# Performance work log

Measured on AMD Instinct MI355X. Metric: run time of the kernel, lower is better.

## Reference

```python
import jax, jax.numpy as jnp
import numpy as np

NN = 128  # number of neighbors (self.nn in the torch module)


def _safe_cdist(A, B):
    # Euclidean pairwise distance with grad-safe sqrt at exact zeros
    sq = (jnp.sum(A * A, -1)[..., :, None]
          + jnp.sum(B * B, -1)[..., None, :]
          - 2.0 * jnp.matmul(A, jnp.swapaxes(B, -1, -2)))
    sq = jnp.maximum(sq, 0.0)
    pos = sq > 0
    return jnp.where(pos, jnp.sqrt(jnp.where(pos, sq, 1.0)), 0.0)


def _kernel(A, B, lv, av):
    # a * exp(-cdist(A/l, B/l) / sqrt(D))
    d = _safe_cdist(A / lv, B / lv) / np.sqrt(A.shape[-1])
    return av * jnp.exp(-d)


def setup_inputs() -> dict:
    key = jax.random.key(0)
    k = jax.random.split(key, 5)
    B, N, D, O = 1024, 100000, 256, 1
    return {
        "x": jax.random.normal(k[0], (B, D), jnp.float32),
        "trainX": jax.random.normal(k[1], (N, D), jnp.float32),
        "trainy": jax.random.normal(k[2], (N, O), jnp.float32),
        "noise": jax.random.normal(k[3], (B, NN, O), jnp.float32),
        "l": jnp.zeros((), jnp.float32),
        "a": jnp.zeros((), jnp.float32),
        "ymean": jnp.zeros((), jnp.float32),
    }


def reference(x, trainX, trainy, noise, l, a, ymean):
    lv = jnp.exp(l)
    av = jnp.exp(a)
    # [B, N] distances, kNN retrieval (eval path: topk of nn, no self-exclusion)
    dists = _safe_cdist(x / lv, trainX / lv)
    _, neighbors = jax.lax.top_k(-dists, NN)          # smallest distances
    nX = trainX[neighbors]                            # [B, NN, D]
    ny = trainy[neighbors] + 0.01 * noise - ymean     # [B, NN, O]
    auto = _kernel(nX, nX, lv, av)                    # [B, NN, NN]
    autoCov = jnp.linalg.inv(auto)                    # batched 128x128 inverse
    crossCov = _kernel(x[:, None, :], nX, lv, av)     # [B, 1, NN]
    kW = crossCov @ autoCov                           # [B, 1, NN]
    y = kW @ ny                                       # [B, 1, O]
    yVar = av * jnp.ones(x.shape[0], x.dtype) - jnp.squeeze(
        kW @ jnp.swapaxes(crossCov, -1, -2))          # [B]
    return (jnp.squeeze(y + ymean, 1), yVar)
```

## Files before the change

kernel.cpp:

```cpp
#include <hip/hip_runtime.h>
#include <math.h>
#include <stdint.h>

#define B_SZ    1024
#define N_TRAIN 100000
#define N_PAD   100096
#define D_DIM   256
#define NN      128
#define KSEL    256
#define CAP     2048
#define NSAMP   1024
#define SRANK   8

typedef unsigned short u16;
typedef unsigned long long u64;
typedef __attribute__((ext_vector_type(8))) short short8v;
typedef __attribute__((ext_vector_type(4))) float f32x4;

__device__ inline u16 f2bf(float f) {
    unsigned u = __float_as_uint(f);
    return (u16)((u + 0x7FFFu + ((u >> 16) & 1u)) >> 16);
}
__device__ inline float bf2f(u16 h) { return __uint_as_float((unsigned)h << 16); }

__global__ __launch_bounds__(256) void k0_norms(const float* __restrict__ trainX,
                                                const float* __restrict__ x,
                                                float* __restrict__ tt,
                                                float* __restrict__ xx) {
    int wave = (blockIdx.x * blockDim.x + threadIdx.x) >> 6;
    int lane = threadIdx.x & 63;
    if (wave >= N_TRAIN + B_SZ) return;
    const float* row = (wave < N_TRAIN) ? (trainX + (size_t)wave * D_DIM)
                                        : (x + (size_t)(wave - N_TRAIN) * D_DIM);
    float4 v = ((const float4*)row)[lane];
    float s = v.x*v.x + v.y*v.y + v.z*v.z + v.w*v.w;
    for (int off = 32; off; off >>= 1) s += __shfl_down(s, off, 64);
    if (lane == 0) { if (wave < N_TRAIN) tt[wave] = s; else xx[wave - N_TRAIN] = s; }
}

__global__ __launch_bounds__(256) void kcv(const float* __restrict__ src,
                                           u16* __restrict__ dst, int n4) {
    int stride = gridDim.x * 256;
    for (int i = blockIdx.x * 256 + threadIdx.x; i < n4; i += stride) {
        float4 v = ((const float4*)src)[i];
        u64 p = (u64)f2bf(v.x) | ((u64)f2bf(v.y) << 16)
              | ((u64)f2bf(v.z) << 32) | ((u64)f2bf(v.w) << 48);
        ((u64*)dst)[i] = p;
    }
}

__global__ __launch_bounds__(256) void kcv2(const float* __restrict__ src,
                                            u16* __restrict__ dstH,
                                            u16* __restrict__ dstL, int n4) {
    int stride = gridDim.x * 256;
    for (int i = blockIdx.x * 256 + threadIdx.x; i < n4; i += stride) {
        float4 v = ((const float4*)src)[i];
        u16 h0 = f2bf(v.x), h1 = f2bf(v.y), h2 = f2bf(v.z), h3 = f2bf(v.w);
        u16 l0 = f2bf(v.x - bf2f(h0)), l1 = f2bf(v.y - bf2f(h1));
        u16 l2 = f2bf(v.z - bf2f(h2)), l3 = f2bf(v.w - bf2f(h3));
        ((u64*)dstH)[i] = (u64)h0 | ((u64)h1 << 16) | ((u64)h2 << 32) | ((u64)h3 << 48);
        ((u64*)dstL)[i] = (u64)l0 | ((u64)l1 << 16) | ((u64)l2 << 32) | ((u64)l3 << 48);
    }
}

__global__ __launch_bounds__(256) void k1m(const u16* __restrict__ Ah,
                                           const u16* __restrict__ Bh,
                                           const float* __restrict__ xx,
                                           const float* __restrict__ tt,
                                           u16* __restrict__ distu,
                                           int row0, int nrows) {
    __shared__ u16 Als[4][128][8];
    __shared__ u16 Bls[4][128][8];
    const int tid = threadIdx.x;
    const int lane = tid & 63, wv = tid >> 6;
    const int wr = wv >> 1, wc = wv & 1;
    const int ib = blockIdx.y * 128;
    const size_t jb = (size_t)blockIdx.x * 128;

    f32x4 acc[4][4];
    #pragma unroll
    for (int m = 0; m < 4; ++m)
        #pragma unroll
        for (int n = 0; n < 4; ++n)
            #pragma unroll
            for (int r = 0; r < 4; ++r) acc[m][n][r] = 0.f;

    for (int k0 = 0; k0 < D_DIM; k0 += 32) {
        #pragma unroll
        for (int r = 0; r < 2; ++r) {
            int c = tid + r * 256;
            int row = c >> 2, ks = c & 3;
            uint4 va = make_uint4(0, 0, 0, 0);
            if (ib + row < nrows)
                va = *(const uint4*)(Ah + (size_t)(row0 + ib + row) * D_DIM + k0 + ks * 8);
            *(uint4*)(&Als[ks][row][0]) = va;
            uint4 vb = make_uint4(0, 0, 0, 0);
            if (jb + row < N_TRAIN)
                vb = *(const uint4*)(Bh + (jb + row) * D_DIM + k0 + ks * 8);
            *(uint4*)(&Bls[ks][row][0]) = vb;
        }
        __syncthreads();
        const int ksl = lane >> 4, li = lane & 15;
        short8v a[4], b[4];
        #pragma unroll
        for (int m = 0; m < 4; ++m)
            a[m] = *(const short8v*)&Als[ksl][wr * 64 + m * 16 + li][0];
        #pragma unroll
        for (int n = 0; n < 4; ++n)
            b[n] = *(const short8v*)&Bls[ksl][wc * 64 + n * 16 + li][0];
        #pragma unroll
        for (int m = 0; m < 4; ++m)
            #pragma unroll
            for (int n = 0; n < 4; ++n)
                acc[m][n] = __builtin_amdgcn_mfma_f32_16x16x32_bf16(a[m], b[n], acc[m][n], 0, 0, 0);
        __syncthreads();
    }
    const int li = lane & 15, lh = lane >> 4;
    float ttv[4]; int cols[4];
    #pragma unroll
    for (int n = 0; n < 4; ++n) {
        cols[n] = (int)jb + wc * 64 + n * 16 + li;
        ttv[n] = (cols[n] < N_TRAIN) ? tt[cols[n]] : 0.f;
    }
    #pragma unroll
    for (int m = 0; m < 4; ++m)
        #pragma unroll
        for (int r = 0; r < 4; ++r) {
            int rl = ib + wr * 64 + m * 16 + lh * 4 + r;
            if (rl >= nrows) continue;
            float xi = xx[row0 + rl];
            u64 pk = 0;
            #pragma unroll
            for (int n = 0; n < 4; ++n) {
                u16 code = 0xFFFFu;
                if (cols[n] < N_TRAIN)
                    code = f2bf(fmaxf(xi + ttv[n] - 2.0f * acc[m][n][r], 0.f));
                pk |= (u64)code << (16 * n);
            }
            *(u64*)(distu + (size_t)rl * N_PAD + jb + wc * 64 + li * 4) = pk;
        }
}

__device__ inline void bitonicU64N(u64* a, int tid, int NE) {
    for (int ks = 2; ks <= NE; ks <<= 1)
        for (int js = ks >> 1; js > 0; js >>= 1) {
            __syncthreads();
            for (int e = tid; e < NE; e += 256) {
                int p = e ^ js;
                if (p > e) {
                    u64 A = a[e], B = a[p];
                    if ((A > B) == ((e & ks) == 0)) { a[e] = B; a[p] = A; }
                }
            }
        }
    __syncthreads();
}
__device__ inline void bitonicU16N(u16* a, int tid, int NE) {
    for (int ks = 2; ks <= NE; ks <<= 1)
        for (int js = ks >> 1; js > 0; js >>= 1) {
            __syncthreads();
            for (int e = tid; e < NE; e += 256) {
                int p = e ^ js;
                if (p > e) {
                    u16 A = a[e], B = a[p];
                    if ((A > B) == ((e & ks) == 0)) { a[e] = B; a[p] = A; }
                }
            }
        }
    __syncthreads();
}

__global__ __launch_bounds__(256) void k2_select(const u16* __restrict__ distu, int row0,
                                                 const float* __restrict__ x,
                                                 const float* __restrict__ trainX,
                                                 const float* __restrict__ xx,
                                                 const float* __restrict__ tt,
                                                 int* __restrict__ nidx,
                                                 float* __restrict__ nsq) {
    const int tid = threadIdx.x;
    const int b = row0 + blockIdx.x;
    const u16* row = distu + (size_t)blockIdx.x * N_PAD;
    const uint4* row8 = (const uint4*)row;
    __shared__ u64 buf[CAP];
    __shared__ int s_cnt;
    __shared__ int sIdx[KSEL];
    __shared__ float4 xs4[64];
    u16* samp = (u16*)buf;

    if (tid < NSAMP / 8) ((uint4*)samp)[tid] = row8[tid];
    __syncthreads();
    bitonicU16N(samp, tid, NSAMP);
    int Tc = (int)samp[SRANK];
    __syncthreads();

    int cnt = 0;
    for (int att = 0; att < 8; ++att) {
        if (tid == 0) s_cnt = 0;
        __syncthreads();
        for (int j8 = tid; j8 < N_PAD / 8; j8 += 256) {
            uint4 v = row8[j8];
            unsigned w_[4] = {v.x, v.y, v.z, v.w};
            #pragma unroll
            for (int c2 = 0; c2 < 4; ++c2) {
                #pragma unroll
                for (int hc = 0; hc < 2; ++hc) {
                    int code = (int)(hc ? (w_[c2] >> 16) : (w_[c2] & 0xFFFFu));
                    if (code < Tc) {
                        int p = atomicAdd(&s_cnt, 1);
                        if (p < CAP) buf[p] = ((u64)(unsigned)code << 32)
                                            | (unsigned)(j8 * 8 + c2 * 2 + hc);
                    }
                }
            }
        }
        __syncthreads();
        cnt = s_cnt;
        if (cnt >= KSEL && cnt <= CAP) break;
        Tc += (cnt < KSEL) ? 8 : -8;
        __syncthreads();
    }
    if (cnt > CAP) cnt = CAP;
    int NE = KSEL;
    while (NE < cnt) NE <<= 1;
    for (int i = tid; i < NE; i += 256) if (i >= cnt) buf[i] = ~0ull;
    __syncthreads();
    bitonicU64N(buf, tid, NE);
    {
        u64 e = buf[tid];
        int jraw = (e == ~0ull) ? 0 : (int)(e & 0xFFFFFFFFull);
        int base = (jraw >> 7) << 7, off = jraw & 127;
        sIdx[tid] = base + (off & 64) + ((off & 3) << 4) + ((off & 63) >> 2);
    }
    if (tid < 64) xs4[tid] = ((const float4*)(x + (size_t)b * D_DIM))[tid];
    __syncthreads();

    const int lane = tid & 63, wv = tid >> 6;
    const int ls = lane & 31;
    const float xxb = xx[b];
    for (int it = 0; it < KSEL / 8; ++it) {
        int c = it * 8 + wv * 2 + (lane >> 5);
        int j = sIdx[c];
        const float4* tr = (const float4*)(trainX + (size_t)j * D_DIM);
        float4 p1 = tr[ls * 2], p2 = tr[ls * 2 + 1];
        float4 q1 = xs4[ls * 2], q2 = xs4[ls * 2 + 1];
        float d = p1.x*q1.x + p1.y*q1.y + p1.z*q1.z + p1.w*q1.w
                + p2.x*q2.x + p2.y*q2.y + p2.z*q2.z + p2.w*q2.w;
        #pragma unroll
        for (int m = 1; m < 32; m <<= 1) d += __shfl_xor(d, m, 64);
        if (ls == 0) {
            float sq = fmaxf(xxb + tt[j] - 2.0f * d, 0.f);
            buf[c] = ((u64)__float_as_uint(sq) << 32) | (unsigned)j;
        }
    }
    __syncthreads();
    bitonicU64N(buf, tid, KSEL);
    if (tid < NN) {
        u64 e = buf[tid];
        nidx[(size_t)b * NN + tid] = (int)(e & 0xFFFFFFFFull);
        nsq[(size_t)b * NN + tid]  = __uint_as_float((unsigned)(e >> 32));
    }
}

__global__ __launch_bounds__(256, 2) void k3_solve(
    const u16* __restrict__ Bh, const u16* __restrict__ Bl,
    const float* __restrict__ trainy,
    const float* __restrict__ noise, const float* __restrict__ tt,
    const int* __restrict__ nidx, const float* __restrict__ nsq,
    const float* __restrict__ lp, const float* __restrict__ ap,
    const float* __restrict__ ymp, float* __restrict__ out) {

    __shared__ u16 Shi[128][40];
    __shared__ u16 Slo[128][40];
    __shared__ float pbuf[2][4][NN];
    __shared__ float diagb[2][4][4];
    __shared__ float yLds[NN], yfwd[NN], dvec[NN], wvec[NN];
    __shared__ int   idxs[NN];
    __shared__ float ttn[NN], c0v[NN];
    __shared__ float red[8];

    const int b = blockIdx.x;
    const int tid = threadIdx.x;
    const int lane = tid & 63, wv = tid >> 6;
    const int wr = wv >> 1, wc = wv & 1;
    const int lr = lane & 15, lq = lane >> 4;

    const float lv = expf(lp[0]);
    const float av = expf(ap[0]);
    const float ymean = ymp[0];
    const float sc = 1.0f / (lv * 16.0f);

    if (tid < NN) {
        int ix = nidx[(size_t)b * NN + tid];
        idxs[tid] = ix;
        ttn[tid] = tt[ix];
        float cc = av * expf(-sqrtf(nsq[(size_t)b * NN + tid]) * sc);
        c0v[tid] = cc;
        yLds[tid] = cc;
    }
    __syncthreads();

    f32x4 acc[4][4];
    #pragma unroll
    for (int m = 0; m < 4; ++m)
        #pragma unroll
        for (int n = 0; n < 4; ++n)
            #pragma unroll
            for (int r = 0; r < 4; ++r) acc[m][n][r] = 0.f;

    for (int c = 0; c < 8; ++c) {
        #pragma unroll
        for (int s = 0; s < 2; ++s) {
            int idx = tid + s * 256;
            int row = idx >> 2, kp = (idx & 3) << 3;
            size_t base = (size_t)idxs[row] * D_DIM + c * 32 + kp;
            *(uint4*)&Shi[row][kp] = *(const uint4*)(Bh + base);
            *(uint4*)&Slo[row][kp] = *(const uint4*)(Bl + base);
        }
        __syncthreads();
        {
            short8v ahi[4], bhi[4];
            #pragma unroll
            for (int m = 0; m < 4; ++m)
                ahi[m] = *(const short8v*)&Shi[wr * 64 + m * 16 + lr][lq * 8];
            #pragma unroll
            for (int n = 0; n < 4; ++n)
                bhi[n] = *(const short8v*)&Shi[wc * 64 + n * 16 + lr][lq * 8];
            #pragma unroll
            for (int m = 0; m < 4; ++m)
                #pragma unroll
                for (int n = 0; n < 4; ++n)
                    acc[m][n] = __builtin_amdgcn_mfma_f32_16x16x32_bf16(ahi[m], bhi[n], acc[m][n], 0, 0, 0);
            #pragma unroll
            for (int n = 0; n < 4; ++n) {
                short8v blo = *(const short8v*)&Slo[wc * 64 + n * 16 + lr][lq * 8];
                #pragma unroll
                for (int m = 0; m < 4; ++m)
                    acc[m][n] = __builtin_amdgcn_mfma_f32_16x16x32_bf16(ahi[m], blo, acc[m][n], 0, 0, 0);
            }
            #pragma unroll
            for (int m = 0; m < 4; ++m) {
                short8v alo = *(const short8v*)&Slo[wr * 64 + m * 16 + lr][lq * 8];
                #pragma unroll
                for (int n = 0; n < 4; ++n)
                    acc[m][n] = __builtin_amdgcn_mfma_f32_16x16x32_bf16(alo, bhi[n], acc[m][n], 0, 0, 0);
            }
        }
        __syncthreads();
    }

    float em[4][4][4];
    #pragma unroll
    for (int m = 0; m < 4; ++m) {
        #pragma unroll
        for (int r = 0; r < 4; ++r) {
            int i = wr * 64 + m * 16 + lq * 4 + r;
            float ti = ttn[i];
            #pragma unroll
            for (int n = 0; n < 4; ++n) {
                int j = wc * 64 + n * 16 + lr;
                float sq = fmaxf(ti + ttn[j] - 2.0f * acc[m][n][r], 0.0f);
                em[m][n][r] = av * expf(-sqrtf(sq) * sc);
            }
        }
    }

    for (int kb = 0; kb < 32; ++kb) {
        const int k0 = kb * 4;
        const int par = kb & 1;
        if (wr == (k0 >> 6) && lq == ((k0 & 15) >> 2)) {
            #pragma unroll
            for (int mm = 0; mm < 4; ++mm)
                if (mm == ((k0 >> 4) & 3)) {
                    #pragma unroll
                    for (int n = 0; n < 4; ++n) {
                        int j = wc * 64 + n * 16 + lr;
                        #pragma unroll
                        for (int r = 0; r < 4; ++r)
                            pbuf[par][r][j] = em[mm][n][r];
                        int cd = j - k0;
                        if (cd >= 0 && cd < 4) {
                            #pragma unroll
                            for (int r = 0; r < 4; ++r)
                                diagb[par][r][cd] = em[mm][n][r];
                        }
                    }
                }
        }
        __syncthreads();
        float d0 = diagb[par][0][0], i0 = 1.0f / d0;
        float B01 = diagb[par][0][1], B02 = diagb[par][0][2], B03 = diagb[par][0][3];
        float l10 = diagb[par][1][0] * i0;
        float l20 = diagb[par][2][0] * i0;
        float l30 = diagb[par][3][0] * i0;
        float d1 = diagb[par][1][1] - l10 * B01, i1 = 1.0f / d1;
        float t12 = diagb[par][1][2] - l10 * B02;
        float t13 = diagb[par][1][3] - l10 * B03;
        float l21 = (diagb[par][2][1] - l20 * B01) * i1;
        float l31 = (diagb[par][3][1] - l30 * B01) * i1;
        float d2 = diagb[par][2][2] - l20 * B02 - l21 * t12, i2 = 1.0f / d2;
        float t23 = diagb[par][2][3] - l20 * B03 - l21 * t13;
        float l32 = (diagb[par][3][2] - l30 * B02 - l31 * t12) * i2;
        float d3 = diagb[par][3][3] - l30 * B03 - l31 * t13 - l32 * t23, i3 = 1.0f / d3;
        if (tid < 128) {
            float a0 = pbuf[par][0][tid];
            float a1 = pbuf[par][1][tid] - l10 * a0;
            float a2 = pbuf[par][2][tid] - l20 * a0 - l21 * a1;
            float a3 = pbuf[par][3][tid] - l30 * a0 - l31 * a1 - l32 * a2;
            pbuf[par][1][tid] = a1;
            pbuf[par][2][tid] = a2;
            pbuf[par][3][tid] = a3;
        }
        __syncthreads();
        #pragma unroll
        for (int r = 0; r < 4; ++r) {
            float ir = (r == 0) ? i0 : (r == 1) ? i1 : (r == 2) ? i2 : i3;
            int kr = k0 + r;
            float cj[4];
            #pragma unroll
            for (int n = 0; n < 4; ++n) {
                int j = wc * 64 + n * 16 + lr;
                cj[n] = (j > kr) ? pbuf[par][r][j] : 0.f;
            }
            #pragma unroll
            for (int m = 0; m < 4; ++m)
                #pragma unroll
                for (int rr = 0; rr < 4; ++rr) {
                    int i = wr * 64 + m * 16 + lq * 4 + rr;
                    float lik = (i > kr) ? pbuf[par][r][i] * ir : 0.f;
                    #pragma unroll
                    for (int n = 0; n < 4; ++n)
                        em[m][n][rr] = fmaf(-lik, cj[n], em[m][n][rr]);
                }
        }
        if (wc == 0 && lr == 0) {
            float fy0 = yLds[k0];
            float fy1 = yLds[k0+1] - l10 * fy0;
            float fy2 = yLds[k0+2] - l20 * fy0 - l21 * fy1;
            float fy3 = yLds[k0+3] - l30 * fy0 - l31 * fy1 - l32 * fy2;
            #pragma unroll
            for (int m = 0; m < 4; ++m)
                #pragma unroll
                for (int rr = 0; rr < 4; ++rr) {
                    int i = wr * 64 + m * 16 + lq * 4 + rr;
                    if (i > k0 + 3) {
                        float yv = yLds[i];
                        yv = fmaf(-pbuf[par][0][i] * i0, fy0, yv);
                        yv = fmaf(-pbuf[par][1][i] * i1, fy1, yv);
                        yv = fmaf(-pbuf[par][2][i] * i2, fy2, yv);
                        yv = fmaf(-pbuf[par][3][i] * i3, fy3, yv);
                        yLds[i] = yv;
                    }
                }
            if (tid == 0) {
                dvec[k0] = d0; dvec[k0+1] = d1; dvec[k0+2] = d2; dvec[k0+3] = d3;
                yfwd[k0] = fy0; yfwd[k0+1] = fy1; yfwd[k0+2] = fy2; yfwd[k0+3] = fy3;
            }
        }
    }
    __syncthreads();
    if (tid < NN) yLds[tid] = yfwd[tid];
    __syncthreads();

    for (int kb = 31; kb >= 0; --kb) {
        const int k0 = kb * 4;
        const int par = kb & 1;
        {
            int q = lr - (k0 & 15);
            if (wc == (k0 >> 6) && q >= 0 && q < 4) {
                #pragma unroll
                for (int nn = 0; nn < 4; ++nn)
                    if (nn == ((k0 >> 4) & 3)) {
                        #pragma unroll
                        for (int m = 0; m < 4; ++m)
                            #pragma unroll
                            for (int r = 0; r < 4; ++r)
                                pbuf[par][q][wr * 64 + m * 16 + lq * 4 + r] = em[m][nn][r];
                    }
            }
        }
        __syncthreads();
        float w3 = yLds[k0+3] / dvec[k0+3];
        float w2 = (yLds[k0+2] - pbuf[par][3][k0+2] * w3) / dvec[k0+2];
        float w1 = (yLds[k0+1] - pbuf[par][2][k0+1] * w2 - pbuf[par][3][k0+1] * w3) / dvec[k0+1];
        float w0 = (yLds[k0]   - pbuf[par][1][k0] * w1 - pbuf[par][2][k0] * w2
                               - pbuf[par][3][k0] * w3) / dvec[k0];
        if (tid == 0) { wvec[k0] = w0; wvec[k0+1] = w1; wvec[k0+2] = w2; wvec[k0+3] = w3; }
        if (tid < k0) {
            float yv = yLds[tid];
            yv = fmaf(-pbuf[par][0][tid], w0, yv);
            yv = fmaf(-pbuf[par][1][tid], w1, yv);
            yv = fmaf(-pbuf[par][2][tid], w2, yv);
            yv = fmaf(-pbuf[par][3][tid], w3, yv);
            yLds[tid] = yv;
        }
    }
    __syncthreads();

    float p1 = 0.f, p2 = 0.f;
    if (tid < NN) {
        float w = wvec[tid];
        float nyv = trainy[idxs[tid]] + 0.01f * noise[(size_t)b * NN + tid] - ymean;
        p1 = w * nyv;
        p2 = w * c0v[tid];
    }
    for (int off = 32; off; off >>= 1) {
        p1 += __shfl_down(p1, off, 64);
        p2 += __shfl_down(p2, off, 64);
    }
    if ((tid & 63) == 0) { red[wv * 2] = p1; red[wv * 2 + 1] = p2; }
    __syncthreads();
    if (tid == 0) {
        out[b]        = (red[0] + red[2] + red[4] + red[6]) + ymean;
        out[B_SZ + b] = av - (red[1] + red[3] + red[5] + red[7]);
    }
}

extern "C" void kernel_launch(void* const* d_in, const int* in_sizes, int n_in,
                              void* d_out, int out_size, void* d_ws, size_t ws_size,
                              hipStream_t stream) {
    const float* x      = (const float*)d_in[0];
    const float* trainX = (const float*)d_in[1];
    const float* trainy = (const float*)d_in[2];
    const float* noise  = (const float*)d_in[3];
    const float* lp     = (const float*)d_in[4];
    const float* ap     = (const float*)d_in[5];
    const float* ymp    = (const float*)d_in[6];
    float* out = (float*)d_out;

    char* ws = (char*)d_ws;
    size_t off = 0;
    auto alloc = [&](size_t bytes) {
        void* p = ws + off;
        off = (off + bytes + 255) & ~(size_t)255;
        return p;
    };
    float* tt   = (float*)alloc((size_t)N_TRAIN * 4);
    float* xx   = (float*)alloc((size_t)B_SZ * 4);
    int*   nidb = (int*)  alloc((size_t)B_SZ * NN * 4);
    float* nsqb = (float*)alloc((size_t)B_SZ * NN * 4);
    u16*   Ah   = (u16*)  alloc((size_t)B_SZ * D_DIM * 2);
    u16*   Bh   = (u16*)  alloc((size_t)N_TRAIN * D_DIM * 2);
    u16*   Bl   = (u16*)  alloc((size_t)N_TRAIN * D_DIM * 2);
    size_t distBytes = (ws_size > off) ? (ws_size - off) : 0;
    u16* distu = (u16*)(ws + off);
    int R = (int)(distBytes / ((size_t)N_PAD * 2));
    if (R > B_SZ) R = B_SZ;
    if (R < 1) R = 1;

    {
        int waves = N_TRAIN + B_SZ;
        k0_norms<<<(waves + 3) / 4, 256, 0, stream>>>(trainX, x, tt, xx);
    }
    kcv2<<<4096, 256, 0, stream>>>(trainX, Bh, Bl, N_TRAIN * D_DIM / 4);
    kcv<<<256, 256, 0, stream>>>(x, Ah, B_SZ * D_DIM / 4);

    for (int r0 = 0; r0 < B_SZ; r0 += R) {
        int rc = (B_SZ - r0 < R) ? (B_SZ - r0) : R;
        dim3 g1((N_TRAIN + 127) / 128, (rc + 127) / 128);
        k1m<<<g1, 256, 0, stream>>>(Ah, Bh, xx, tt, distu, r0, rc);
        k2_select<<<rc, 256, 0, stream>>>(distu, r0, x, trainX, xx, tt, nidb, nsqb);
    }
    k3_solve<<<B_SZ, 256, 0, stream>>>(Bh, Bl, trainy, noise, tt, nidb, nsqb,
                                       lp, ap, ymp, out);
}
```

Measured before the change: 776.0 us.

## Fuse norm and bf16 split prep kernels; transpose panel buffer for vector LDS access

Merges the row-norm kernel and the two bf16 hi/lo conversion kernels into one pass, so trainX is read once instead of twice and two launches go away. In the batched LDL solve, the shared panel buffer is transposed to [NN][4] so each row's four pivot-column values load and store as one float4. The rank-4 trailing update is reorganised into a fused four-FMA chain per element. This cuts LDS instruction count in the inner loop, at the cost of possible bank conflicts with the new 16-byte stride pattern.

```diff
diff --git a/kernel.cpp b/kernel.cpp
--- a/kernel.cpp
+++ b/kernel.cpp
@@ -23,43 +23,34 @@
 }
 __device__ inline float bf2f(u16 h) { return __uint_as_float((unsigned)h << 16); }
 
-__global__ __launch_bounds__(256) void k0_norms(const float* __restrict__ trainX,
-                                                const float* __restrict__ x,
-                                                float* __restrict__ tt,
-                                                float* __restrict__ xx) {
+__global__ __launch_bounds__(256) void kprep(const float* __restrict__ trainX,
+                                             const float* __restrict__ x,
+                                             float* __restrict__ tt,
+                                             float* __restrict__ xx,
+                                             u16* __restrict__ Bh,
+                                             u16* __restrict__ Bl,
+                                             u16* __restrict__ Ah) {
     int wave = (blockIdx.x * blockDim.x + threadIdx.x) >> 6;
     int lane = threadIdx.x & 63;
     if (wave >= N_TRAIN + B_SZ) return;
-    const float* row = (wave < N_TRAIN) ? (trainX + (size_t)wave * D_DIM)
-                                        : (x + (size_t)(wave - N_TRAIN) * D_DIM);
+    const bool isTrain = wave < N_TRAIN;
+    const float* row = isTrain ? (trainX + (size_t)wave * D_DIM)
+                               : (x + (size_t)(wave - N_TRAIN) * D_DIM);
     float4 v = ((const float4*)row)[lane];
     float s = v.x*v.x + v.y*v.y + v.z*v.z + v.w*v.w;
     for (int off = 32; off; off >>= 1) s += __shfl_down(s, off, 64);
-    if (lane == 0) { if (wave < N_TRAIN) tt[wave] = s; else xx[wave - N_TRAIN] = s; }
-}
-
-__global__ __launch_bounds__(256) void kcv(const float* __restrict__ src,
-                                           u16* __restrict__ dst, int n4) {
-    int stride = gridDim.x * 256;
-    for (int i = blockIdx.x * 256 + threadIdx.x; i < n4; i += stride) {
-        float4 v = ((const float4*)src)[i];
-        u64 p = (u64)f2bf(v.x) | ((u64)f2bf(v.y) << 16)
-              | ((u64)f2bf(v.z) << 32) | ((u64)f2bf(v.w) << 48);
-        ((u64*)dst)[i] = p;
-    }
-}
-
-__global__ __launch_bounds__(256) void kcv2(const float* __restrict__ src,
-                                            u16* __restrict__ dstH,
-                                            u16* __restrict__ dstL, int n4) {
-    int stride = gridDim.x * 256;
-    for (int i = blockIdx.x * 256 + threadIdx.x; i < n4; i += stride) {
-        float4 v = ((const float4*)src)[i];
-        u16 h0 = f2bf(v.x), h1 = f2bf(v.y), h2 = f2bf(v.z), h3 = f2bf(v.w);
+    u16 h0 = f2bf(v.x), h1 = f2bf(v.y), h2 = f2bf(v.z), h3 = f2bf(v.w);
+    u64 hp = (u64)h0 | ((u64)h1 << 16) | ((u64)h2 << 32) | ((u64)h3 << 48);
+    if (isTrain) {
+        ((u64*)(Bh + (size_t)wave * D_DIM))[lane] = hp;
         u16 l0 = f2bf(v.x - bf2f(h0)), l1 = f2bf(v.y - bf2f(h1));
         u16 l2 = f2bf(v.z - bf2f(h2)), l3 = f2bf(v.w - bf2f(h3));
-        ((u64*)dstH)[i] = (u64)h0 | ((u64)h1 << 16) | ((u64)h2 << 32) | ((u64)h3 << 48);
-        ((u64*)dstL)[i] = (u64)l0 | ((u64)l1 << 16) | ((u64)l2 << 32) | ((u64)l3 << 48);
+        ((u64*)(Bl + (size_t)wave * D_DIM))[lane] =
+            (u64)l0 | ((u64)l1 << 16) | ((u64)l2 << 32) | ((u64)l3 << 48);
+        if (lane == 0) tt[wave] = s;
+    } else {
+        ((u64*)(Ah + (size_t)(wave - N_TRAIN) * D_DIM))[lane] = hp;
+        if (lane == 0) xx[wave - N_TRAIN] = s;
     }
 }
 
@@ -271,7 +262,7 @@
 
     __shared__ u16 Shi[128][40];
     __shared__ u16 Slo[128][40];
-    __shared__ float pbuf[2][4][NN];
+    __shared__ __align__(16) float pbufT[2][NN][4];
     __shared__ float diagb[2][4][4];
     __shared__ float yLds[NN], yfwd[NN], dvec[NN], wvec[NN];
     __shared__ int   idxs[NN];
@@ -374,9 +365,8 @@
                     #pragma unroll
                     for (int n = 0; n < 4; ++n) {
                         int j = wc * 64 + n * 16 + lr;
-                        #pragma unroll
-                        for (int r = 0; r < 4; ++r)
-                            pbuf[par][r][j] = em[mm][n][r];
+                        *(float4*)&pbufT[par][j][0] =
+                            make_float4(em[mm][n][0], em[mm][n][1], em[mm][n][2], em[mm][n][3]);
                         int cd = j - k0;
                         if (cd >= 0 && cd < 4) {
                             #pragma unroll
@@ -402,36 +392,44 @@
         float l32 = (diagb[par][3][2] - l30 * B02 - l31 * t12) * i2;
         float d3 = diagb[par][3][3] - l30 * B03 - l31 * t13 - l32 * t23, i3 = 1.0f / d3;
         if (tid < 128) {
-            float a0 = pbuf[par][0][tid];
-            float a1 = pbuf[par][1][tid] - l10 * a0;
-            float a2 = pbuf[par][2][tid] - l20 * a0 - l21 * a1;
-            float a3 = pbuf[par][3][tid] - l30 * a0 - l31 * a1 - l32 * a2;
-            pbuf[par][1][tid] = a1;
-            pbuf[par][2][tid] = a2;
-            pbuf[par][3][tid] = a3;
-        }
-        __syncthreads();
-        #pragma unroll
-        for (int r = 0; r < 4; ++r) {
-            float ir = (r == 0) ? i0 : (r == 1) ? i1 : (r == 2) ? i2 : i3;
-            int kr = k0 + r;
-            float cj[4];
-            #pragma unroll
-            for (int n = 0; n < 4; ++n) {
-                int j = wc * 64 + n * 16 + lr;
-                cj[n] = (j > kr) ? pbuf[par][r][j] : 0.f;
-            }
-            #pragma unroll
-            for (int m = 0; m < 4; ++m)
-                #pragma unroll
-                for (int rr = 0; rr < 4; ++rr) {
-                    int i = wr * 64 + m * 16 + lq * 4 + rr;
-                    float lik = (i > kr) ? pbuf[par][r][i] * ir : 0.f;
-                    #pragma unroll
-                    for (int n = 0; n < 4; ++n)
-                        em[m][n][rr] = fmaf(-lik, cj[n], em[m][n][rr]);
+            float4 a = *(const float4*)&pbufT[par][tid][0];
+            float a1 = a.y - l10 * a.x;
+            float a2 = a.z - l20 * a.x - l21 * a1;
+            float a3 = a.w - l30 * a.x - l31 * a1 - l32 * a2;
+            a.y = a1; a.z = a2; a.w = a3;
+            *(float4*)&pbufT[par][tid][0] = a;
+        }
+        __syncthreads();
+        float cj0[4], cj1[4], cj2[4], cj3[4];
+        #pragma unroll
+        for (int n = 0; n < 4; ++n) {
+            int j = wc * 64 + n * 16 + lr;
+            float4 cv = *(const float4*)&pbufT[par][j][0];
+            cj0[n] = (j > k0)     ? cv.x : 0.f;
+            cj1[n] = (j > k0 + 1) ? cv.y : 0.f;
+            cj2[n] = (j > k0 + 2) ? cv.z : 0.f;
+            cj3[n] = (j > k0 + 3) ? cv.w : 0.f;
+        }
+        #pragma unroll
+        for (int m = 0; m < 4; ++m)
+            #pragma unroll
+            for (int rr = 0; rr < 4; ++rr) {
+                int i = wr * 64 + m * 16 + lq * 4 + rr;
+                float4 rv = *(const float4*)&pbufT[par][i][0];
+                float k0v = (i > k0)     ? rv.x * i0 : 0.f;
+                float k1v = (i > k0 + 1) ? rv.y * i1 : 0.f;
+                float k2v = (i > k0 + 2) ? rv.z * i2 : 0.f;
+                float k3v = (i > k0 + 3) ? rv.w * i3 : 0.f;
+                #pragma unroll
+                for (int n = 0; n < 4; ++n) {
+                    float t = em[m][n][rr];
+                    t = fmaf(-k0v, cj0[n], t);
+                    t = fmaf(-k1v, cj1[n], t);
+                    t = fmaf(-k2v, cj2[n], t);
+                    t = fmaf(-k3v, cj3[n], t);
+                    em[m][n][rr] = t;
                 }
-        }
+            }
         if (wc == 0 && lr == 0) {
             float fy0 = yLds[k0];
             float fy1 = yLds[k0+1] - l10 * fy0;
@@ -443,11 +441,12 @@
                 for (int rr = 0; rr < 4; ++rr) {
                     int i = wr * 64 + m * 16 + lq * 4 + rr;
                     if (i > k0 + 3) {
+                        float4 rv = *(const float4*)&pbufT[par][i][0];
                         float yv = yLds[i];
-                        yv = fmaf(-pbuf[par][0][i] * i0, fy0, yv);
-                        yv = fmaf(-pbuf[par][1][i] * i1, fy1, yv);
-                        yv = fmaf(-pbuf[par][2][i] * i2, fy2, yv);
-                        yv = fmaf(-pbuf[par][3][i] * i3, fy3, yv);
+                        yv = fmaf(-rv.x * i0, fy0, yv);
+                        yv = fmaf(-rv.y * i1, fy1, yv);
+                        yv = fmaf(-rv.z * i2, fy2, yv);
+                        yv = fmaf(-rv.w * i3, fy3, yv);
                         yLds[i] = yv;
                     }
                 }
@@ -474,23 +473,24 @@
                         for (int m = 0; m < 4; ++m)
                             #pragma unroll
                             for (int r = 0; r < 4; ++r)
-                                pbuf[par][q][wr * 64 + m * 16 + lq * 4 + r] = em[m][nn][r];
+                                pbufT[par][wr * 64 + m * 16 + lq * 4 + r][q] = em[m][nn][r];
                     }
             }
         }
         __syncthreads();
         float w3 = yLds[k0+3] / dvec[k0+3];
-        float w2 = (yLds[k0+2] - pbuf[par][3][k0+2] * w3) / dvec[k0+2];
-        float w1 = (yLds[k0+1] - pbuf[par][2][k0+1] * w2 - pbuf[par][3][k0+1] * w3) / dvec[k0+1];
-        float w0 = (yLds[k0]   - pbuf[par][1][k0] * w1 - pbuf[par][2][k0] * w2
-                               - pbuf[par][3][k0] * w3) / dvec[k0];
+        float w2 = (yLds[k0+2] - pbufT[par][k0+2][3] * w3) / dvec[k0+2];
+        float w1 = (yLds[k0+1] - pbufT[par][k0+1][2] * w2 - pbufT[par][k0+1][3] * w3) / dvec[k0+1];
+        float w0 = (yLds[k0]   - pbufT[par][k0][1] * w1 - pbufT[par][k0][2] * w2
+                               - pbufT[par][k0][3] * w3) / dvec[k0];
         if (tid == 0) { wvec[k0] = w0; wvec[k0+1] = w1; wvec[k0+2] = w2; wvec[k0+3] = w3; }
         if (tid < k0) {
+            float4 pv = *(const float4*)&pbufT[par][tid][0];
             float yv = yLds[tid];
-            yv = fmaf(-pbuf[par][0][tid], w0, yv);
-            yv = fmaf(-pbuf[par][1][tid], w1, yv);
-            yv = fmaf(-pbuf[par][2][tid], w2, yv);
-            yv = fmaf(-pbuf[par][3][tid], w3, yv);
+            yv = fmaf(-pv.x, w0, yv);
+            yv = fmaf(-pv.y, w1, yv);
+            yv = fmaf(-pv.z, w2, yv);
+            yv = fmaf(-pv.w, w3, yv);
             yLds[tid] = yv;
         }
     }
@@ -549,10 +549,8 @@
 
     {
         int waves = N_TRAIN + B_SZ;
-        k0_norms<<<(waves + 3) / 4, 256, 0, stream>>>(trainX, x, tt, xx);
-    }
-    kcv2<<<4096, 256, 0, stream>>>(trainX, Bh, Bl, N_TRAIN * D_DIM / 4);
-    kcv<<<256, 256, 0, stream>>>(x, Ah, B_SZ * D_DIM / 4);
+        kprep<<<(waves + 3) / 4, 256, 0, stream>>>(trainX, x, tt, xx, Bh, Bl, Ah);
+    }
 
     for (int r0 = 0; r0 < B_SZ; r0 += R) {
         int rc = (B_SZ - r0 < R) ? (B_SZ - r0) : R;
```

Result: faster. 627.8 us (median of 4 runs) (-19.1%).
